# Kernel optimization log

Hardware: AMD Instinct MI355X
Metric: run time of the kernel (lower is better)

## Reference

```python
import jax, jax.numpy as jnp
import numpy as np
import math

D = 768; H = 12; DH = D // H; FF = 3072; B = 8; S = 512
D_K_NEIGHBOR = 64.0
EPS = 1e-5

def _linear(x, W, b):
    return x @ W + b

def _layernorm(x, g, b):
    m = jnp.mean(x, axis=-1, keepdims=True)
    v = jnp.var(x, axis=-1, keepdims=True)
    return (x - m) * jax.lax.rsqrt(v + EPS) * g + b

def setup_inputs():
    key = jax.random.key(0)
    ks = jax.random.split(key, 24)
    w = lambda k, shape: (0.02 * jax.random.normal(k, shape)).astype(jnp.float32)
    z = lambda n: jnp.zeros((n,), jnp.float32)
    return {
        'x': jax.random.normal(ks[0], (B, S, D), dtype=jnp.float32),
        'src_padding_mask': jnp.ones((B, S), dtype=bool),
        'prev_affinity_scores_a': jax.random.uniform(ks[1], (B, S - 1), dtype=jnp.float32),
        'Wqn': w(ks[2], (D, D)), 'bqn': z(D),
        'Wkn': w(ks[3], (D, D)), 'bkn': z(D),
        'Wq': w(ks[4], (D, D)), 'bq': z(D),
        'Wk': w(ks[5], (D, D)), 'bk': z(D),
        'Wv': w(ks[6], (D, D)), 'bv': z(D),
        'Wo': w(ks[7], (D, D)), 'bo': z(D),
        'W1': w(ks[8], (D, FF)), 'b1': z(FF),
        'W2': w(ks[9], (FF, D)), 'b2': z(D),
        'g1': jnp.ones((D,), jnp.float32), 'be1': z(D),
        'g2': jnp.ones((D,), jnp.float32), 'be2': z(D),
        'layer_idx': 0,
    }

def _affinity(x, Wqn, bqn, Wkn, bkn, prev_a, layer_idx):
    q = _linear(x, Wqn, bqn)  # [B,S,D]
    k = _linear(x, Wkn, bkn)
    s_fwd = jnp.sum(q[:, :-1] * k[:, 1:], axis=-1) / D_K_NEIGHBOR  # [B,S-1]
    s_bwd = jnp.sum(q[:, 1:] * k[:, :-1], axis=-1) / D_K_NEIGHBOR
    a_hat = (jax.nn.sigmoid(s_fwd) + jax.nn.sigmoid(s_bwd)) * 0.5
    if layer_idx == 0:
        return a_hat
    return prev_a + (1.0 - prev_a) * a_hat

def _mask_C(a):
    # C[b,i,j] = prod_{t=min(i,j)}^{max(i,j)-1} a[b,t]; diag = 1.
    # Log-space prefix sums replace the O(S^2) python loop of the original:
    # L[k] = sum_{t<k} log a[t]; C[i,j] = exp(L[max(i,j)] - L[min(i,j)]).
    L = jnp.concatenate([jnp.zeros((a.shape[0], 1), a.dtype),
                         jnp.cumsum(jnp.log(a), axis=1)], axis=1)  # [B,S]
    ii = jnp.arange(S)
    imin = jnp.minimum(ii[:, None], ii[None, :])
    imax = jnp.maximum(ii[:, None], ii[None, :])
    C = jnp.exp(L[:, imax] - L[:, imin])  # [B,S,S]
    return C[:, None]  # [B,1,S,S]

def reference(x, src_padding_mask, prev_affinity_scores_a, Wqn, bqn, Wkn, bkn,
              Wq, bq, Wk, bk, Wv, bv, Wo, bo, W1, b1, W2, b2, g1, be1, g2, be2,
              layer_idx):
    a = _affinity(x, Wqn, bqn, Wkn, bkn, prev_affinity_scores_a, layer_idx)
    C = _mask_C(a)
    residual = x
    xn = _layernorm(x, g1, be1)
    q = _linear(xn, Wq, bq).reshape(B, S, H, DH).transpose(0, 2, 1, 3)
    k = _linear(xn, Wk, bk).reshape(B, S, H, DH).transpose(0, 2, 1, 3)
    v = _linear(xn, Wv, bv).reshape(B, S, H, DH).transpose(0, 2, 1, 3)
    scores = jnp.einsum('bhqd,bhkd->bhqk', q, k) / math.sqrt(DH)
    scores = jnp.where(src_padding_mask[:, None, None, :], scores, -1e9)
    attn = jax.nn.softmax(scores, axis=-1)
    attn_h = C * attn  # hierarchical masking of attention weights
    ctx = jnp.einsum('bhqk,bhkd->bhqd', attn_h, v)
    ctx = ctx.transpose(0, 2, 1, 3).reshape(B, S, D)
    x1 = residual + _linear(ctx, Wo, bo)
    xn2 = _layernorm(x1, g2, be2)
    ffn = _linear(jax.nn.relu(_linear(xn2, W1, b1)), W2, b2)
    out = x1 + ffn
    return out, a, attn_h
```

## Files before the change

kernel.cpp:

```cpp
#include <hip/hip_runtime.h>
#include <math.h>

#define B_  8
#define S_  512
#define D_  768
#define H_  12
#define DH_ 64
#define FF_ 3072
#define M_  (B_ * S_)

typedef unsigned short u16;
typedef unsigned int   u32;
typedef __bf16  bf16x8 __attribute__((ext_vector_type(8)));
typedef float   f32x4  __attribute__((ext_vector_type(4)));
typedef unsigned short u16x4 __attribute__((ext_vector_type(4)));

__device__ __forceinline__ float b2f(u16 h) {
    union { u32 u; float f; } v; v.u = ((u32)h) << 16; return v.f;
}
__device__ __forceinline__ u16 f2b(float f) {
    union { u32 u; float f; } v; v.f = f;
    u32 u = v.u;
    u32 r = (u + 0x7FFFu + ((u >> 16) & 1u)) >> 16;
    return (u16)r;
}

__device__ __forceinline__ void gload16(const void* g, void* l) {
    __builtin_amdgcn_global_load_lds(
        (const __attribute__((address_space(1))) void*)g,
        (__attribute__((address_space(3))) void*)l, 16, 0, 0);
}

__global__ void cast_f32_bf16(const float* __restrict__ X, u16* __restrict__ Y, int n4) {
    int i4 = (blockIdx.x * 256 + threadIdx.x);
    if (i4 >= n4) return;
    f32x4 v = *(const f32x4*)(X + (size_t)i4 * 4);
    u16x4 o;
    o.x = f2b(v.x); o.y = f2b(v.y); o.z = f2b(v.z); o.w = f2b(v.w);
    *(u16x4*)(Y + (size_t)i4 * 4) = o;
}

__global__ void prefill_bias(const float* __restrict__ res, const float* __restrict__ bias,
                             float* __restrict__ out, int N, int n4) {
    int i4 = blockIdx.x * 256 + threadIdx.x;
    if (i4 >= n4) return;
    int base = i4 * 4;
    int col = base % N;
    f32x4 r = *(const f32x4*)(res + base);
    f32x4 bv = *(const f32x4*)(bias + col);
    r.x += bv.x; r.y += bv.y; r.z += bv.z; r.w += bv.w;
    *(f32x4*)(out + base) = r;
}

__global__ void transpose_cast(const float* __restrict__ W, u16* __restrict__ WT,
                               int R, int C) {
    __shared__ u16 tile[32][33];
    int c0 = blockIdx.x * 32;
    int r0 = blockIdx.y * 32;
    int tx = threadIdx.x, ty = threadIdx.y;
    #pragma unroll
    for (int j = 0; j < 32; j += 8)
        tile[ty + j][tx] = f2b(W[(size_t)(r0 + ty + j) * C + (c0 + tx)]);
    __syncthreads();
    #pragma unroll
    for (int j = 0; j < 32; j += 8)
        WT[(size_t)(c0 + ty + j) * R + (r0 + tx)] = tile[tx][ty + j];
}

__launch_bounds__(256)
__global__ void gemm_mfma(const u16* __restrict__ A, const u16* __restrict__ BT,
                          const float* __restrict__ bias, const float* __restrict__ res,
                          u16* __restrict__ Cb, float* __restrict__ Cf,
                          int N, int K, int klen, int relu, int split)
{
    __shared__ __align__(16) u16 As[128 * 64];
    __shared__ __align__(16) u16 Bs[128 * 64];
    int tid = threadIdx.x;
    int wave = tid >> 6, lane = tid & 63;
    int m0 = blockIdx.y * 128, n0 = blockIdx.x * 128;
    int kbeg = blockIdx.z * klen;
    int wm = (wave >> 1) * 64, wn = (wave & 1) * 64;
    int r16 = lane & 15, kq = lane >> 4;
    f32x4 acc[4][4] = {};
    for (int k0 = 0; k0 < klen; k0 += 64) {
        #pragma unroll
        for (int i = 0; i < 4; ++i) {
            int cid = i * 256 + tid;
            int row = cid >> 3, phys = cid & 7, logc = phys ^ (row & 7);
            gload16(&A [(size_t)(m0 + row) * K + kbeg + k0 + logc * 8], &As[cid * 8]);
            gload16(&BT[(size_t)(n0 + row) * K + kbeg + k0 + logc * 8], &Bs[cid * 8]);
        }
        __syncthreads();
        #pragma unroll
        for (int ks = 0; ks < 2; ++ks) {
            bf16x8 af[4], bfr[4];
            #pragma unroll
            for (int i = 0; i < 4; ++i) {
                int row = wm + i * 16 + r16;
                af[i] = *(const bf16x8*)&As[row * 64 + (((ks * 4 + kq) ^ (row & 7)) * 8)];
            }
            #pragma unroll
            for (int j = 0; j < 4; ++j) {
                int row = wn + j * 16 + r16;
                bfr[j] = *(const bf16x8*)&Bs[row * 64 + (((ks * 4 + kq) ^ (row & 7)) * 8)];
            }
            #pragma unroll
            for (int i = 0; i < 4; ++i)
                #pragma unroll
                for (int j = 0; j < 4; ++j)
                    acc[i][j] = __builtin_amdgcn_mfma_f32_16x16x32_bf16(
                        af[i], bfr[j], acc[i][j], 0, 0, 0);
        }
        __syncthreads();
    }
    if (split) {
        #pragma unroll
        for (int i = 0; i < 4; ++i) {
            int rg = m0 + wm + i * 16 + kq * 4;
            #pragma unroll
            for (int j = 0; j < 4; ++j) {
                int cg = n0 + wn + j * 16 + r16;
                #pragma unroll
                for (int r = 0; r < 4; ++r)
                    atomicAdd(&Cf[(size_t)(rg + r) * N + cg], acc[i][j][r]);
            }
        }
        return;
    }
    #pragma unroll
    for (int i = 0; i < 4; ++i) {
        int rg = m0 + wm + i * 16 + kq * 4;
        #pragma unroll
        for (int j = 0; j < 4; ++j) {
            int cg = n0 + wn + j * 16 + r16;
            float bc = bias[cg];
            #pragma unroll
            for (int r = 0; r < 4; ++r) {
                float v = acc[i][j][r] + bc;
                if (relu) v = fmaxf(v, 0.f);
                size_t off = (size_t)(rg + r) * N + cg;
                if (res) v += res[off];
                if (Cb) Cb[off] = f2b(v);
                if (Cf) Cf[off] = v;
            }
        }
    }
}

__global__ void affinity_k(const u16* __restrict__ nk,
                           const float* __restrict__ prev, const int* __restrict__ lidx,
                           float* __restrict__ a_out)
{
    const int ST = 2 * D_;
    int gid  = blockIdx.x * 4 + (threadIdx.x >> 6);
    int lane = threadIdx.x & 63;
    if (gid >= B_ * (S_ - 1)) return;
    int b = gid / (S_ - 1), i = gid % (S_ - 1);
    const u16* q0 = nk + (size_t)(b * S_ + i)     * ST;
    const u16* q1 = nk + (size_t)(b * S_ + i + 1) * ST;
    const u16* k0 = q0 + D_;
    const u16* k1 = q1 + D_;
    float sf = 0.f, sb = 0.f;
    for (int d = lane; d < D_; d += 64) {
        sf += b2f(q0[d]) * b2f(k1[d]);
        sb += b2f(q1[d]) * b2f(k0[d]);
    }
    #pragma unroll
    for (int off = 32; off > 0; off >>= 1) {
        sf += __shfl_xor(sf, off);
        sb += __shfl_xor(sb, off);
    }
    if (lane == 0) {
        sf *= (1.f / 64.f); sb *= (1.f / 64.f);
        float ah = 0.5f * (1.f / (1.f + expf(-sf)) + 1.f / (1.f + expf(-sb)));
        float a = ah;
        if (lidx[0] != 0) { float p = prev[gid]; a = p + (1.f - p) * ah; }
        a_out[gid] = a;
    }
}

__global__ void cumsum_k(const float* __restrict__ a_f, float* __restrict__ L) {
    int b = blockIdx.x;
    int lane = threadIdx.x;
    float lg[8]; float s = 0.f;
    #pragma unroll
    for (int r = 0; r < 8; ++r) {
        int t = lane * 8 + r;
        lg[r] = (t < S_ - 1) ? logf(fmaxf(a_f[b * (S_ - 1) + t], 1e-35f)) : 0.f;
        s += lg[r];
    }
    float incl = s;
    #pragma unroll
    for (int off = 1; off < 64; off <<= 1) {
        float n = __shfl_up(incl, off);
        if (lane >= off) incl += n;
    }
    float run = incl - s;
    #pragma unroll
    for (int r = 0; r < 8; ++r) {
        L[b * S_ + lane * 8 + r] = run;
        run += lg[r];
    }
}

__global__ void layernorm_k(const float* __restrict__ X, const float* __restrict__ g,
                            const float* __restrict__ be, u16* __restrict__ Y)
{
    int row  = blockIdx.x * 4 + (threadIdx.x >> 6);
    int lane = threadIdx.x & 63;
    const float* xr = X + (size_t)row * D_;
    float xs[12], s = 0.f, sq = 0.f;
    #pragma unroll
    for (int t = 0; t < 12; ++t) {
        float v = xr[lane + t * 64];
        xs[t] = v; s += v; sq += v * v;
    }
    #pragma unroll
    for (int off = 32; off > 0; off >>= 1) {
        s  += __shfl_xor(s, off);
        sq += __shfl_xor(sq, off);
    }
    float m  = s  * (1.f / (float)D_);
    float var = sq * (1.f / (float)D_) - m * m;
    float rs = rsqrtf(var + 1e-5f);
    u16* yr = Y + (size_t)row * D_;
    #pragma unroll
    for (int t = 0; t < 12; ++t) {
        int d = lane + t * 64;
        yr[d] = f2b((xs[t] - m) * rs * g[d] + be[d]);
    }
}

__global__ void vt_transpose(const u16* __restrict__ QKV, u16* __restrict__ Vt) {
    const int ST = 3 * D_;
    __shared__ u16 tile[32][33];
    int bh = blockIdx.z; int b = bh / H_, h = bh % H_;
    int j0 = blockIdx.x * 32;
    int d0 = blockIdx.y * 32;
    int tx = threadIdx.x, ty = threadIdx.y;
    #pragma unroll
    for (int jj = 0; jj < 32; jj += 8)
        tile[ty + jj][tx] = QKV[(size_t)(b * S_ + j0 + ty + jj) * ST + 2 * D_ + h * DH_ + d0 + tx];
    __syncthreads();
    #pragma unroll
    for (int jj = 0; jj < 32; jj += 8)
        Vt[((size_t)bh * DH_ + d0 + ty + jj) * S_ + (j0 + tx)] = tile[tx][ty + jj];
}

__launch_bounds__(256, 2)
__global__ void qk_softmax_c(const u16* __restrict__ QKV, const float* __restrict__ L,
                             float* __restrict__ Attn)
{
    const int ST = 3 * D_;
    __shared__ __align__(16) u16 Ks[S_ * 64];
    __shared__ __align__(16) u16 Qs[64 * 64];
    __shared__ float Lsh[S_];
    int bh = blockIdx.y; int b = bh / H_, h = bh % H_;
    int q0 = blockIdx.x * 64;
    int tid = threadIdx.x;
    int wave = tid >> 6, lane = tid & 63;
    int r16 = lane & 15, kq = lane >> 4;
    #pragma unroll
    for (int i = 0; i < 2; ++i) {
        int cid = i * 256 + tid;
        int row = cid >> 3, phys = cid & 7, logc = phys ^ (row & 7);
        *(bf16x8*)&Qs[row * 64 + phys * 8] =
            *(const bf16x8*)&QKV[(size_t)(b * S_ + q0 + row) * ST + h * DH_ + logc * 8];
    }
    #pragma unroll
    for (int i = 0; i < 16; ++i) {
        int cid = i * 256 + tid;
        int row = cid >> 3, phys = cid & 7, logc = phys ^ (row & 7);
        *(bf16x8*)&Ks[row * 64 + phys * 8] =
            *(const bf16x8*)&QKV[(size_t)(b * S_ + row) * ST + D_ + h * DH_ + logc * 8];
    }
    for (int j = tid; j < S_; j += 256) Lsh[j] = L[b * S_ + j];
    __syncthreads();
    int arow = wave * 16 + r16;
    bf16x8 a0 = *(const bf16x8*)&Qs[arow * 64 + (((kq)     ^ (arow & 7)) * 8)];
    bf16x8 a1 = *(const bf16x8*)&Qs[arow * 64 + (((4 + kq) ^ (arow & 7)) * 8)];
    f32x4 acc[32];
    #pragma unroll
    for (int jt = 0; jt < 32; ++jt) {
        int brow = jt * 16 + r16;
        bf16x8 b0 = *(const bf16x8*)&Ks[brow * 64 + (((kq)     ^ (brow & 7)) * 8)];
        bf16x8 b1 = *(const bf16x8*)&Ks[brow * 64 + (((4 + kq) ^ (brow & 7)) * 8)];
        f32x4 z = {0.f, 0.f, 0.f, 0.f};
        z = __builtin_amdgcn_mfma_f32_16x16x32_bf16(a0, b0, z, 0, 0, 0);
        acc[jt] = __builtin_amdgcn_mfma_f32_16x16x32_bf16(a1, b1, z, 0, 0, 0);
    }
    float mxv[4] = {-1e30f, -1e30f, -1e30f, -1e30f};
    #pragma unroll
    for (int jt = 0; jt < 32; ++jt)
        #pragma unroll
        for (int r = 0; r < 4; ++r)
            mxv[r] = fmaxf(mxv[r], acc[jt][r] * 0.125f);
    #pragma unroll
    for (int mk = 1; mk <= 8; mk <<= 1)
        #pragma unroll
        for (int r = 0; r < 4; ++r)
            mxv[r] = fmaxf(mxv[r], __shfl_xor(mxv[r], mk));
    float sum[4] = {0.f, 0.f, 0.f, 0.f};
    #pragma unroll
    for (int jt = 0; jt < 32; ++jt)
        #pragma unroll
        for (int r = 0; r < 4; ++r) {
            float e = expf(acc[jt][r] * 0.125f - mxv[r]);
            acc[jt][r] = e; sum[r] += e;
        }
    #pragma unroll
    for (int mk = 1; mk <= 8; mk <<= 1)
        #pragma unroll
        for (int r = 0; r < 4; ++r)
            sum[r] += __shfl_xor(sum[r], mk);
    float inv[4], Lq[4]; int qrow[4];
    #pragma unroll
    for (int r = 0; r < 4; ++r) {
        inv[r] = 1.f / sum[r];
        qrow[r] = q0 + wave * 16 + kq * 4 + r;
        Lq[r] = Lsh[qrow[r]];
    }
    size_t obase = (size_t)bh * S_ * S_;
    #pragma unroll
    for (int jt = 0; jt < 32; ++jt) {
        int j = jt * 16 + r16;
        float Lj = Lsh[j];
        #pragma unroll
        for (int r = 0; r < 4; ++r) {
            float d = (j >= qrow[r]) ? (Lj - Lq[r]) : (Lq[r] - Lj);
            float pv = acc[jt][r] * inv[r] * expf(fminf(d, 0.f));
            Attn[obase + (size_t)qrow[r] * S_ + j] = pv;
        }
    }
}

__launch_bounds__(256)
__global__ void av_mfma(const float* __restrict__ Attn, const u16* __restrict__ Vt,
                        u16* __restrict__ ctx)
{
    const int LP = 136;
    __shared__ __align__(16) u16 Ps[128 * LP];
    __shared__ __align__(16) u16 Vs[64 * LP];
    int bh = blockIdx.y; int b = bh / H_, h = bh % H_;
    int q0 = blockIdx.x * 128;
    int tid = threadIdx.x;
    int wave = tid >> 6, lane = tid & 63;
    int wq = wave * 32;
    int r16 = lane & 15, kq = lane >> 4;
    f32x4 acc[2][4] = {};
    size_t abase = ((size_t)bh * S_ + q0) * S_;
    const u16* vtb = Vt + (size_t)bh * DH_ * S_;
    int prow = tid >> 1, pcb = (tid & 1) * 64;
    int vrow = tid >> 2, vcb = (tid & 3) * 32;
    for (int jc = 0; jc < S_; jc += 128) {
        {
            const float* pg = Attn + abase + (size_t)prow * S_ + jc + pcb;
            u16* pl = &Ps[prow * LP + pcb];
            #pragma unroll
            for (int c = 0; c < 8; ++c) {
                f32x4 a = *(const f32x4*)(pg + c * 8);
                f32x4 bvv = *(const f32x4*)(pg + c * 8 + 4);
                u16 tmp[8];
                tmp[0]=f2b(a.x); tmp[1]=f2b(a.y); tmp[2]=f2b(a.z); tmp[3]=f2b(a.w);
                tmp[4]=f2b(bvv.x); tmp[5]=f2b(bvv.y); tmp[6]=f2b(bvv.z); tmp[7]=f2b(bvv.w);
                *(u16x4*)(pl + c * 8)     = *(u16x4*)&tmp[0];
                *(u16x4*)(pl + c * 8 + 4) = *(u16x4*)&tmp[4];
            }
        }
        {
            const u16* vg = vtb + (size_t)vrow * S_ + jc + vcb;
            u16* vl = &Vs[vrow * LP + vcb];
            #pragma unroll
            for (int c = 0; c < 4; ++c)
                *(bf16x8*)(vl + c * 8) = *(const bf16x8*)(vg + c * 8);
        }
        __syncthreads();
        #pragma unroll
        for (int ks = 0; ks < 4; ++ks) {
            bf16x8 af[2], bfr[4];
            #pragma unroll
            for (int i = 0; i < 2; ++i)
                af[i] = *(const bf16x8*)&Ps[(wq + i * 16 + r16) * LP + ks * 32 + kq * 8];
            #pragma unroll
            for (int n = 0; n < 4; ++n)
                bfr[n] = *(const bf16x8*)&Vs[(n * 16 + r16) * LP + ks * 32 + kq * 8];
            #pragma unroll
            for (int i = 0; i < 2; ++i)
                #pragma unroll
                for (int n = 0; n < 4; ++n)
                    acc[i][n] = __builtin_amdgcn_mfma_f32_16x16x32_bf16(
                        af[i], bfr[n], acc[i][n], 0, 0, 0);
        }
        __syncthreads();
    }
    #pragma unroll
    for (int i = 0; i < 2; ++i) {
        int qg = q0 + wq + i * 16 + kq * 4;
        #pragma unroll
        for (int n = 0; n < 4; ++n) {
            int d = n * 16 + r16;
            #pragma unroll
            for (int r = 0; r < 4; ++r)
                ctx[(size_t)(b * S_ + qg + r) * D_ + h * DH_ + d] = f2b(acc[i][n][r]);
        }
    }
}

extern "C" void kernel_launch(void* const* d_in, const int* in_sizes, int n_in,
                              void* d_out, int out_size, void* d_ws, size_t ws_size,
                              hipStream_t stream) {
    const float* x    = (const float*)d_in[0];
    const float* prev = (const float*)d_in[2];
    const float* Wqn = (const float*)d_in[3];  const float* bqn = (const float*)d_in[4];
    const float* Wkn = (const float*)d_in[5];  const float* bkn = (const float*)d_in[6];
    const float* Wq  = (const float*)d_in[7];  const float* bq  = (const float*)d_in[8];
    const float* Wk  = (const float*)d_in[9];  const float* bk  = (const float*)d_in[10];
    const float* Wv  = (const float*)d_in[11]; const float* bv  = (const float*)d_in[12];
    const float* Wo  = (const float*)d_in[13]; const float* bo  = (const float*)d_in[14];
    const float* W1  = (const float*)d_in[15]; const float* b1  = (const float*)d_in[16];
    const float* W2  = (const float*)d_in[17]; const float* b2  = (const float*)d_in[18];
    const float* g1  = (const float*)d_in[19]; const float* be1 = (const float*)d_in[20];
    const float* g2  = (const float*)d_in[21]; const float* be2 = (const float*)d_in[22];
    const int* lidx = (const int*)d_in[23];

    char* ws = (char*)d_ws;
    size_t off = 0;
    auto alloc = [&](size_t bytes) -> void* {
        void* p = ws + off; off += (bytes + 255) & ~(size_t)255; return p;
    };
    const size_t DDe = (size_t)D_ * D_;
    u16* WT_nk  = (u16*)alloc(2 * DDe * 2);
    u16* WT_qkv = (u16*)alloc(3 * DDe * 2);
    u16* WT_o   = (u16*)alloc(DDe * 2);
    u16* W1T    = (u16*)alloc((size_t)FF_ * D_ * 2);
    u16* W2T    = (u16*)alloc((size_t)FF_ * D_ * 2);
    float* bias_nk  = (float*)alloc(2 * D_ * 4);
    float* bias_qkv = (float*)alloc(3 * D_ * 4);
    u16* xb    = (u16*)alloc((size_t)M_ * D_ * 2);
    u16* nk_b  = (u16*)alloc((size_t)M_ * 2 * D_ * 2);
    u16* qkv_b = (u16*)alloc((size_t)M_ * 3 * D_ * 2);
    float* L_f = (float*)alloc((size_t)B_ * S_ * 4);
    u16* xn_b  = (u16*)alloc((size_t)M_ * D_ * 2);
    u16* ctx_b = (u16*)alloc((size_t)M_ * D_ * 2);
    float* x1_f = (float*)alloc((size_t)M_ * D_ * 4);
    u16* h_b = nk_b;
    u16* xn2_b = xn_b;
    u16* Vt = xb;

    float* out0     = (float*)d_out;
    float* out_a    = out0 + (size_t)M_ * D_;
    float* out_attn = out_a + (size_t)B_ * (S_ - 1);

    dim3 tb(32, 8);
    cast_f32_bf16<<<(M_ * D_ / 4 + 255) / 256, 256, 0, stream>>>(x, xb, M_ * D_ / 4);
    transpose_cast<<<dim3(D_/32, D_/32), tb, 0, stream>>>(Wqn, WT_nk,            D_, D_);
    transpose_cast<<<dim3(D_/32, D_/32), tb, 0, stream>>>(Wkn, WT_nk + DDe,      D_, D_);
    transpose_cast<<<dim3(D_/32, D_/32), tb, 0, stream>>>(Wq,  WT_qkv,           D_, D_);
    transpose_cast<<<dim3(D_/32, D_/32), tb, 0, stream>>>(Wk,  WT_qkv + DDe,     D_, D_);
    transpose_cast<<<dim3(D_/32, D_/32), tb, 0, stream>>>(Wv,  WT_qkv + 2 * DDe, D_, D_);
    transpose_cast<<<dim3(D_/32, D_/32), tb, 0, stream>>>(Wo,  WT_o,             D_, D_);
    transpose_cast<<<dim3(FF_/32, D_/32), tb, 0, stream>>>(W1, W1T, D_, FF_);
    transpose_cast<<<dim3(D_/32, FF_/32), tb, 0, stream>>>(W2, W2T, FF_, D_);
    hipMemcpyAsync(bias_nk,         bqn, D_ * 4, hipMemcpyDeviceToDevice, stream);
    hipMemcpyAsync(bias_nk + D_,    bkn, D_ * 4, hipMemcpyDeviceToDevice, stream);
    hipMemcpyAsync(bias_qkv,        bq,  D_ * 4, hipMemcpyDeviceToDevice, stream);
    hipMemcpyAsync(bias_qkv + D_,   bk,  D_ * 4, hipMemcpyDeviceToDevice, stream);
    hipMemcpyAsync(bias_qkv + 2*D_, bv,  D_ * 4, hipMemcpyDeviceToDevice, stream);

    gemm_mfma<<<dim3(2*D_/128, M_/128), 256, 0, stream>>>(
        xb, WT_nk, bias_nk, nullptr, nk_b, nullptr, 2*D_, D_, D_, 0, 0);
    affinity_k<<<(B_ * (S_ - 1) + 3) / 4, 256, 0, stream>>>(nk_b, prev, lidx, out_a);
    cumsum_k<<<B_, 64, 0, stream>>>(out_a, L_f);

    layernorm_k<<<M_ / 4, 256, 0, stream>>>(x, g1, be1, xn_b);
    gemm_mfma<<<dim3(3*D_/128, M_/128), 256, 0, stream>>>(
        xn_b, WT_qkv, bias_qkv, nullptr, qkv_b, nullptr, 3*D_, D_, D_, 0, 0);

    vt_transpose<<<dim3(S_/32, DH_/32, B_*H_), tb, 0, stream>>>(qkv_b, Vt);
    qk_softmax_c<<<dim3(S_/64, B_*H_), 256, 0, stream>>>(qkv_b, L_f, out_attn);
    av_mfma<<<dim3(S_/128, B_*H_), 256, 0, stream>>>(out_attn, Vt, ctx_b);

    prefill_bias<<<(M_ * D_ / 4 + 255) / 256, 256, 0, stream>>>(x, bo, x1_f, D_, M_ * D_ / 4);
    gemm_mfma<<<dim3(D_/128, M_/128, 2), 256, 0, stream>>>(
        ctx_b, WT_o, nullptr, nullptr, nullptr, x1_f, D_, D_, D_/2, 0, 1);
    layernorm_k<<<M_ / 4, 256, 0, stream>>>(x1_f, g2, be2, xn2_b);
    gemm_mfma<<<dim3(FF_/128, M_/128), 256, 0, stream>>>(
        xn2_b, W1T, b1, nullptr, h_b, nullptr, FF_, D_, D_, 1, 0);
    prefill_bias<<<(M_ * D_ / 4 + 255) / 256, 256, 0, stream>>>(x1_f, b2, out0, D_, M_ * D_ / 4);
    gemm_mfma<<<dim3(D_/128, M_/128, 4), 256, 0, stream>>>(
        h_b, W2T, nullptr, nullptr, nullptr, out0, D_, FF_, FF_/4, 0, 1);
}
```

Baseline: 507.4 us.

## Replace split-K atomics with partial buffers and reduce kernel; batch weight transposes

Split-K GEMMs now write their partial sums to a separate per-split buffer with plain stores, and a new reduce kernel adds residual, bias and all partials in one pass. This replaces the prefill-plus-atomicAdd scheme, whose float atomics to global memory are costly. The six square weight transposes are merged into one launch, and the five bias memcpys become a single kernel, which cuts launch overhead. In exchange the change needs an extra 4×M×D float workspace and writes then re-reads the partials, which adds memory traffic.

```diff
diff --git a/kernel.cpp b/kernel.cpp
--- a/kernel.cpp
+++ b/kernel.cpp
@@ -40,16 +40,25 @@
     *(u16x4*)(Y + (size_t)i4 * 4) = o;
 }
 
-__global__ void prefill_bias(const float* __restrict__ res, const float* __restrict__ bias,
-                             float* __restrict__ out, int N, int n4) {
-    int i4 = blockIdx.x * 256 + threadIdx.x;
-    if (i4 >= n4) return;
-    int base = i4 * 4;
-    int col = base % N;
-    f32x4 r = *(const f32x4*)(res + base);
-    f32x4 bv = *(const f32x4*)(bias + col);
-    r.x += bv.x; r.y += bv.y; r.z += bv.z; r.w += bv.w;
-    *(f32x4*)(out + base) = r;
+__global__ void transpose6(const float* s0, const float* s1, const float* s2,
+                           const float* s3, const float* s4, const float* s5,
+                           u16* d0, u16* d1, u16* d2, u16* d3, u16* d4, u16* d5)
+{
+    __shared__ u16 tile[32][33];
+    int z = blockIdx.z;
+    const float* W = (z == 0) ? s0 : (z == 1) ? s1 : (z == 2) ? s2
+                   : (z == 3) ? s3 : (z == 4) ? s4 : s5;
+    u16* WT = (z == 0) ? d0 : (z == 1) ? d1 : (z == 2) ? d2
+            : (z == 3) ? d3 : (z == 4) ? d4 : d5;
+    int c0 = blockIdx.x * 32, r0 = blockIdx.y * 32;
+    int tx = threadIdx.x, ty = threadIdx.y;
+    #pragma unroll
+    for (int j = 0; j < 32; j += 8)
+        tile[ty + j][tx] = f2b(W[(size_t)(r0 + ty + j) * D_ + (c0 + tx)]);
+    __syncthreads();
+    #pragma unroll
+    for (int j = 0; j < 32; j += 8)
+        WT[(size_t)(c0 + ty + j) * D_ + (r0 + tx)] = tile[tx][ty + j];
 }
 
 __global__ void transpose_cast(const float* __restrict__ W, u16* __restrict__ WT,
@@ -65,6 +74,18 @@
     #pragma unroll
     for (int j = 0; j < 32; j += 8)
         WT[(size_t)(c0 + ty + j) * R + (r0 + tx)] = tile[tx][ty + j];
+}
+
+__global__ void bias_concat(const float* bqn, const float* bkn, const float* bq,
+                            const float* bk, const float* bv,
+                            float* bias_nk, float* bias_qkv)
+{
+    int i = blockIdx.x * 256 + threadIdx.x;
+    if (i < 768)       bias_nk[i] = bqn[i];
+    else if (i < 1536) bias_nk[i] = bkn[i - 768];
+    else if (i < 2304) bias_qkv[i - 1536] = bq[i - 1536];
+    else if (i < 3072) bias_qkv[i - 1536] = bk[i - 2304];
+    else if (i < 3840) bias_qkv[i - 1536] = bv[i - 3072];
 }
 
 __launch_bounds__(256)
@@ -114,6 +135,7 @@
         __syncthreads();
     }
     if (split) {
+        float* Pf = Cf + (size_t)blockIdx.z * M_ * N;
         #pragma unroll
         for (int i = 0; i < 4; ++i) {
             int rg = m0 + wm + i * 16 + kq * 4;
@@ -122,7 +144,7 @@
                 int cg = n0 + wn + j * 16 + r16;
                 #pragma unroll
                 for (int r = 0; r < 4; ++r)
-                    atomicAdd(&Cf[(size_t)(rg + r) * N + cg], acc[i][j][r]);
+                    Pf[(size_t)(rg + r) * N + cg] = acc[i][j][r];
             }
         }
         return;
@@ -145,6 +167,25 @@
             }
         }
     }
+}
+
+__global__ void reduce_k(const float* __restrict__ parts, int KS,
+                         const float* __restrict__ res, const float* __restrict__ bias,
+                         float* __restrict__ out, int N, int n4)
+{
+    int i4 = blockIdx.x * 256 + threadIdx.x;
+    if (i4 >= n4) return;
+    size_t base = (size_t)i4 * 4;
+    int col = (int)(base % N);
+    f32x4 acc = *(const f32x4*)(res + base);
+    f32x4 bv = *(const f32x4*)(bias + col);
+    acc.x += bv.x; acc.y += bv.y; acc.z += bv.z; acc.w += bv.w;
+    const size_t MN = (size_t)M_ * N;
+    for (int s = 0; s < KS; ++s) {
+        f32x4 p = *(const f32x4*)(parts + s * MN + base);
+        acc.x += p.x; acc.y += p.y; acc.z += p.z; acc.w += p.w;
+    }
+    *(f32x4*)(out + base) = acc;
 }
 
 __global__ void affinity_k(const u16* __restrict__ nk,
@@ -443,6 +484,7 @@
     u16* xn_b  = (u16*)alloc((size_t)M_ * D_ * 2);
     u16* ctx_b = (u16*)alloc((size_t)M_ * D_ * 2);
     float* x1_f = (float*)alloc((size_t)M_ * D_ * 4);
+    float* parts = (float*)alloc((size_t)4 * M_ * D_ * 4);
     u16* h_b = nk_b;
     u16* xn2_b = xn_b;
     u16* Vt = xb;
@@ -453,19 +495,12 @@
 
     dim3 tb(32, 8);
     cast_f32_bf16<<<(M_ * D_ / 4 + 255) / 256, 256, 0, stream>>>(x, xb, M_ * D_ / 4);
-    transpose_cast<<<dim3(D_/32, D_/32), tb, 0, stream>>>(Wqn, WT_nk,            D_, D_);
-    transpose_cast<<<dim3(D_/32, D_/32), tb, 0, stream>>>(Wkn, WT_nk + DDe,      D_, D_);
-    transpose_cast<<<dim3(D_/32, D_/32), tb, 0, stream>>>(Wq,  WT_qkv,           D_, D_);
-    transpose_cast<<<dim3(D_/32, D_/32), tb, 0, stream>>>(Wk,  WT_qkv + DDe,     D_, D_);
-    transpose_cast<<<dim3(D_/32, D_/32), tb, 0, stream>>>(Wv,  WT_qkv + 2 * DDe, D_, D_);
-    transpose_cast<<<dim3(D_/32, D_/32), tb, 0, stream>>>(Wo,  WT_o,             D_, D_);
+    transpose6<<<dim3(D_/32, D_/32, 6), tb, 0, stream>>>(
+        Wqn, Wkn, Wq, Wk, Wv, Wo,
+        WT_nk, WT_nk + DDe, WT_qkv, WT_qkv + DDe, WT_qkv + 2 * DDe, WT_o);
     transpose_cast<<<dim3(FF_/32, D_/32), tb, 0, stream>>>(W1, W1T, D_, FF_);
     transpose_cast<<<dim3(D_/32, FF_/32), tb, 0, stream>>>(W2, W2T, FF_, D_);
-    hipMemcpyAsync(bias_nk,         bqn, D_ * 4, hipMemcpyDeviceToDevice, stream);
-    hipMemcpyAsync(bias_nk + D_,    bkn, D_ * 4, hipMemcpyDeviceToDevice, stream);
-    hipMemcpyAsync(bias_qkv,        bq,  D_ * 4, hipMemcpyDeviceToDevice, stream);
-    hipMemcpyAsync(bias_qkv + D_,   bk,  D_ * 4, hipMemcpyDeviceToDevice, stream);
-    hipMemcpyAsync(bias_qkv + 2*D_, bv,  D_ * 4, hipMemcpyDeviceToDevice, stream);
+    bias_concat<<<15, 256, 0, stream>>>(bqn, bkn, bq, bk, bv, bias_nk, bias_qkv);
 
     gemm_mfma<<<dim3(2*D_/128, M_/128), 256, 0, stream>>>(
         xb, WT_nk, bias_nk, nullptr, nk_b, nullptr, 2*D_, D_, D_, 0, 0);
@@ -480,13 +515,15 @@
     qk_softmax_c<<<dim3(S_/64, B_*H_), 256, 0, stream>>>(qkv_b, L_f, out_attn);
     av_mfma<<<dim3(S_/128, B_*H_), 256, 0, stream>>>(out_attn, Vt, ctx_b);
 
-    prefill_bias<<<(M_ * D_ / 4 + 255) / 256, 256, 0, stream>>>(x, bo, x1_f, D_, M_ * D_ / 4);
     gemm_mfma<<<dim3(D_/128, M_/128, 2), 256, 0, stream>>>(
-        ctx_b, WT_o, nullptr, nullptr, nullptr, x1_f, D_, D_, D_/2, 0, 1);
+        ctx_b, WT_o, nullptr, nullptr, nullptr, parts, D_, D_, D_/2, 0, 1);
+    reduce_k<<<(M_ * D_ / 4 + 255) / 256, 256, 0, stream>>>(
+        parts, 2, x, bo, x1_f, D_, M_ * D_ / 4);
     layernorm_k<<<M_ / 4, 256, 0, stream>>>(x1_f, g2, be2, xn2_b);
     gemm_mfma<<<dim3(FF_/128, M_/128), 256, 0, stream>>>(
         xn2_b, W1T, b1, nullptr, h_b, nullptr, FF_, D_, D_, 1, 0);
-    prefill_bias<<<(M_ * D_ / 4 + 255) / 256, 256, 0, stream>>>(x1_f, b2, out0, D_, M_ * D_ / 4);
     gemm_mfma<<<dim3(D_/128, M_/128, 4), 256, 0, stream>>>(
-        h_b, W2T, nullptr, nullptr, nullptr, out0, D_, FF_, FF_/4, 0, 1);
-}
+        h_b, W2T, nullptr, nullptr, nullptr, parts, D_, FF_, FF_/4, 0, 1);
+    reduce_k<<<(M_ * D_ / 4 + 255) / 256, 256, 0, stream>>>(
+        parts, 4, x1_f, b2, out0, D_, M_ * D_ / 4);
+}
```

After: 455.7 us. -10.2%, faster.
